# Performance work log

Measured on AMD Instinct MI355X. Metric: run time of the kernel, lower is better.

The kernel has to match this reference:

```python
import jax, jax.numpy as jnp
import numpy as np
import math

B, L, D, P = 2, 2048, 256, 32
PI = math.pi


def _layernorm(x, g, b, eps=1e-5):
    m = x.mean(-1, keepdims=True)
    v = x.var(-1, keepdims=True)
    return (x - m) / jnp.sqrt(v + eps) * g + b


def setup_inputs() -> dict:
    key = jax.random.key(0)
    ks = jax.random.split(key, 16)
    sd = 1.0 / math.sqrt(D)
    f32 = jnp.float32
    inp = {
        "x": jax.random.normal(ks[0], (B, L, D), f32),
        # key_encoder: Linear(D, P)
        "key_W": jax.random.normal(ks[1], (D, P), f32) * sd,
        "key_b": jnp.zeros((P,), f32),
        # value_encoder: Linear(D, D)
        "val_W": jax.random.normal(ks[2], (D, D), f32) * sd,
        "val_b": jnp.zeros((D,), f32),
        # refiner: LayerNorm(D), Linear(D, 2D), GELU, Linear(2D, D)
        "ln1_g": jnp.ones((D,), f32),
        "ln1_b": jnp.zeros((D,), f32),
        "W1": jax.random.normal(ks[3], (D, 2 * D), f32) * sd,
        "b1": jnp.zeros((2 * D,), f32),
        "W2": jax.random.normal(ks[4], (2 * D, D), f32) * (1.0 / math.sqrt(2 * D)),
        "b2": jnp.zeros((D,), f32),
        # to_out: LayerNorm(D), Linear(D, D)
        "ln2_g": jnp.ones((D,), f32),
        "ln2_b": jnp.zeros((D,), f32),
        "Wo": jax.random.normal(ks[5], (D, D), f32) * sd,
        "bo": jnp.zeros((D,), f32),
    }
    return inp


def reference(x, key_W, key_b, val_W, val_b, ln1_g, ln1_b, W1, b1, W2, b2,
              ln2_g, ln2_b, Wo, bo):
    # key phases in (-pi, pi); phasor exp(i*theta) handled as (cos, sin)
    phases = jnp.tanh(x @ key_W + key_b) * PI          # (B, L, P)
    values = x @ val_W + val_b                          # (B, L, D)

    cos_p = jnp.cos(phases)
    sin_p = jnp.sin(phases)
    # torch.roll(shifts=1, dims=1) then zero the first position -> shift right, row 0 = 0
    zrow = jnp.zeros_like(cos_p[:, :1])
    cos_s = jnp.concatenate([zrow, cos_p[:, :-1]], axis=1)
    sin_s = jnp.concatenate([zrow, sin_p[:, :-1]], axis=1)

    # odd positions hold values
    vmask = (jnp.arange(L) % 2 == 1).astype(x.dtype)    # (L,)
    mv = values * vmask[None, :, None]                  # (B, L, D)

    # bind: outer product phasor (P) x value (D); real/imag parts
    bound_re = cos_s[..., None] * mv[:, :, None, :]     # (B, L, P, D)
    bound_im = sin_s[..., None] * mv[:, :, None, :]
    mem_re = jnp.cumsum(bound_re, axis=1)
    mem_im = jnp.cumsum(bound_im, axis=1)

    # retrieve: Re[ memory * exp(-i*theta) ] summed over phases
    retrieved = (jnp.einsum('blpd,blp->bld', mem_re, cos_p)
                 + jnp.einsum('blpd,blp->bld', mem_im, sin_p))

    valid = jnp.maximum(jnp.cumsum(vmask), 1.0)         # (L,)
    retrieved = retrieved / (jnp.sqrt(valid)[None, :, None] * math.sqrt(P))

    h = _layernorm(retrieved, ln1_g, ln1_b)
    h = jax.nn.gelu(h @ W1 + b1, approximate=False)
    refined = h @ W2 + b2
    out = x + (_layernorm(refined, ln2_g, ln2_b) @ Wo + bo)
    return out
```

## Files before the change

### kernel.cpp

```cpp
#include <hip/hip_runtime.h>
#include <math.h>

#define BB 2
#define LL 2048
#define DD 256
#define PP 32
#define NC 64
#define PI_F 3.14159265358979323846f

typedef __attribute__((ext_vector_type(8))) short bf16x8;
typedef __attribute__((ext_vector_type(4))) float f32x4;
typedef unsigned short ushort_t;
typedef unsigned int uint_t;

__device__ inline ushort_t f2bf(float x) {
    uint_t u = __float_as_uint(x);
    uint_t r = (u + 0x7fffu + ((u >> 16) & 1u)) >> 16;
    return (ushort_t)r;
}

__global__ __launch_bounds__(256) void prep_key_kernel(
    const float* __restrict__ W1, const float* __restrict__ W2,
    const float* __restrict__ Wo, const float* __restrict__ valW,
    const float* __restrict__ x, const float* __restrict__ key_W,
    const float* __restrict__ key_b,
    ushort_t* __restrict__ W1t, ushort_t* __restrict__ W2t,
    ushort_t* __restrict__ Wot, ushort_t* __restrict__ valWt,
    float2* __restrict__ ph)
{
    const int bid = blockIdx.x;
    const int t = threadIdx.x;
    if (bid < 96) {
        __shared__ float T[64][65];
        const float* W; ushort_t* Wt; int K, N, tile;
        if (bid < 32)      { W = W1;   Wt = W1t;   K = 256; N = 512; tile = bid; }
        else if (bid < 64) { W = W2;   Wt = W2t;   K = 512; N = 256; tile = bid - 32; }
        else if (bid < 80) { W = Wo;   Wt = Wot;   K = 256; N = 256; tile = bid - 64; }
        else               { W = valW; Wt = valWt; K = 256; N = 256; tile = bid - 80; }
        const int ntiles = N / 64;
        const int k0 = (tile / ntiles) * 64, n0 = (tile % ntiles) * 64;
        {
            const int rr = t >> 2, cb = (t & 3) * 16;
            #pragma unroll
            for (int i = 0; i < 16; i += 4) {
                const float4 v = *(const float4*)&W[(k0 + rr) * N + n0 + cb + i];
                T[rr][cb + i + 0] = v.x; T[rr][cb + i + 1] = v.y;
                T[rr][cb + i + 2] = v.z; T[rr][cb + i + 3] = v.w;
            }
        }
        __syncthreads();
        {
            const int n = t >> 2, kb = (t & 3) * 16;
            #pragma unroll
            for (int i = 0; i < 16; ++i)
                Wt[(n0 + n) * K + k0 + kb + i] = f2bf(T[kb + i][n]);
        }
    } else {
        __shared__ float xs[256][8];
        __shared__ float kw[256][33];
        const int row0 = (bid - 96) * 8;
        #pragma unroll
        for (int i = 0; i < 8; ++i)
            xs[t][i] = x[(row0 + i) * DD + t];
        #pragma unroll
        for (int p4 = 0; p4 < 8; ++p4) {
            const int idx4 = p4 * 256 + t;
            const int k = idx4 >> 3, pc = (idx4 & 7) * 4;
            const float4 v = *(const float4*)&key_W[k * 32 + pc];
            kw[k][pc + 0] = v.x; kw[k][pc + 1] = v.y;
            kw[k][pc + 2] = v.z; kw[k][pc + 3] = v.w;
        }
        __syncthreads();
        const int r = t >> 5, p = t & 31;
        float a = key_b[p];
        #pragma unroll 8
        for (int k = 0; k < DD; ++k)
            a += xs[k][r] * kw[k][p];
        a = tanhf(a) * PI_F;
        float sn, cs;
        sincosf(a, &sn, &cs);
        ph[(row0 + r) * PP + p] = make_float2(cs, sn);
    }
}

__global__ __launch_bounds__(256) void valbind_kernel(
    const float* __restrict__ x, const float2* __restrict__ ph,
    const ushort_t* __restrict__ valWt, const float* __restrict__ val_b,
    ushort_t* __restrict__ VoddT, float* __restrict__ Mt)
{
    __shared__ ushort_t xsb[16][264];
    __shared__ ushort_t VdT[128][40];
    __shared__ ushort_t phsT[64][40];
    __shared__ float    Ms[128][68];

    const int tid = threadIdx.x;
    const int bid = blockIdx.x;
    const int b  = bid >> 7;
    const int rem = bid & 127;
    const int c  = rem >> 1;
    const int dh = rem & 1;
    const int base = b * LL;
    const int r0 = 32 * c;

    {
        const int j = tid >> 4, cb = (tid & 15) * 16;
        const float* src = &x[(long)(base + r0 + 2 * j + 1) * DD + cb];
        ushort_t tmp[16];
        #pragma unroll
        for (int i = 0; i < 4; ++i) {
            const float4 v = *(const float4*)&src[i * 4];
            tmp[i*4+0] = f2bf(v.x); tmp[i*4+1] = f2bf(v.y);
            tmp[i*4+2] = f2bf(v.z); tmp[i*4+3] = f2bf(v.w);
        }
        *(uint4*)&xsb[j][cb]     = *(uint4*)&tmp[0];
        *(uint4*)&xsb[j][cb + 8] = *(uint4*)&tmp[8];
    }
    {
        const int j = tid >> 4, qb = (tid & 15) * 4;
        const float4 v = *(const float4*)((const float*)ph +
                              (long)(base + r0 + 2 * j) * 64 + qb);
        phsT[qb + 0][j] = f2bf(v.x);
        phsT[qb + 1][j] = f2bf(v.y);
        phsT[qb + 2][j] = f2bf(v.z);
        phsT[qb + 3][j] = f2bf(v.w);
    }
    for (int e = tid; e < 64 * 16; e += 256)
        phsT[e >> 4][16 + (e & 15)] = 0;
    for (int e = tid; e < 128 * 16; e += 256)
        VdT[e >> 4][16 + (e & 15)] = 0;
    __syncthreads();

    const int wv = tid >> 6, lane = tid & 63;
    const int qd = lane >> 4, mc = lane & 15;

    f32x4 va0 = {0.f,0.f,0.f,0.f}, va1 = {0.f,0.f,0.f,0.f};
    const int dloc0 = wv * 32 + mc, dloc1 = dloc0 + 16;
    const int n0g = dh * 128 + dloc0, n1g = n0g + 16;
    const ushort_t* B0 = &valWt[(long)n0g * 256];
    const ushort_t* B1 = &valWt[(long)n1g * 256];
    #pragma unroll
    for (int ks = 0; ks < 8; ++ks) {
        const bf16x8 a  = *(const bf16x8*)&xsb[mc][ks * 32 + qd * 8];
        const bf16x8 b0 = *(const bf16x8*)&B0[ks * 32 + qd * 8];
        const bf16x8 b1 = *(const bf16x8*)&B1[ks * 32 + qd * 8];
        va0 = __builtin_amdgcn_mfma_f32_16x16x32_bf16(a, b0, va0, 0, 0, 0);
        va1 = __builtin_amdgcn_mfma_f32_16x16x32_bf16(a, b1, va1, 0, 0, 0);
    }
    {
        const float bb0 = val_b[n0g], bb1 = val_b[n1g];
        #pragma unroll
        for (int r = 0; r < 4; ++r) {
            const int j = qd * 4 + r;
            VdT[dloc0][j] = f2bf(va0[r] + bb0);
            VdT[dloc1][j] = f2bf(va1[r] + bb1);
        }
    }
    __syncthreads();

    const bf16x8 a2 = *(const bf16x8*)&phsT[wv * 16 + mc][qd * 8];
    f32x4 macc[8];
    #pragma unroll
    for (int nf = 0; nf < 8; ++nf) {
        f32x4 z = {0.f,0.f,0.f,0.f};
        const bf16x8 b2 = *(const bf16x8*)&VdT[nf * 16 + mc][qd * 8];
        macc[nf] = __builtin_amdgcn_mfma_f32_16x16x32_bf16(a2, b2, z, 0, 0, 0);
    }
    #pragma unroll
    for (int nf = 0; nf < 8; ++nf) {
        #pragma unroll
        for (int r = 0; r < 4; ++r) {
            const int q = wv * 16 + qd * 4 + r;
            Ms[nf * 16 + mc][q] = macc[nf][r];
        }
    }
    __syncthreads();

    {
        float* dst = &Mt[((long)(b * NC + c) * 256 + dh * 128) * 64];
        #pragma unroll
        for (int p = 0; p < 8; ++p) {
            const int idx4 = p * 256 + tid;
            const int dloc = idx4 >> 4, q4 = (idx4 & 15) * 4;
            const float4 v = *(const float4*)&Ms[dloc][q4];
            *(float4*)&dst[dloc * 64 + q4] = v;
        }
    }
    if (tid < 128) {
        ushort_t* vd = &VoddT[((long)(b * NC + c) * 256 + dh * 128 + tid) * 16];
        *(uint4*)&vd[0] = *(const uint4*)&VdT[tid][0];
        *(uint4*)&vd[8] = *(const uint4*)&VdT[tid][8];
    }
}

__global__ __launch_bounds__(256) void prefix_kernel(float* __restrict__ M)
{
    __shared__ float segsum[4][64];
    const int tid = threadIdx.x;
    const int b  = blockIdx.x >> 8;
    const int cg = blockIdx.x & 255;
    const int col = cg * 64 + (tid & 63);
    const int seg = tid >> 6;
    const long base = (long)b * NC * 16384 + col;

    float v[16], s = 0.f;
    #pragma unroll
    for (int i = 0; i < 16; ++i) {
        v[i] = M[base + (long)(seg * 16 + i) * 16384];
        s += v[i];
    }
    segsum[seg][tid & 63] = s;
    __syncthreads();
    float run = 0.f;
    #pragma unroll
    for (int sg = 0; sg < 3; ++sg)
        if (sg < seg) run += segsum[sg][tid & 63];
    #pragma unroll
    for (int i = 0; i < 16; ++i) {
        const long a = base + (long)(seg * 16 + i) * 16384;
        M[a] = run;
        run += v[i];
    }
}

__global__ __launch_bounds__(256) void retrieve_kernel(
    const float* __restrict__ ph, const float* __restrict__ Mpre,
    const ushort_t* __restrict__ VoddT,
    const float* __restrict__ ln1_g, const float* __restrict__ ln1_b,
    ushort_t* __restrict__ rhat)
{
    __shared__ ushort_t Bs_m[256][72];
    __shared__ ushort_t Bs_v[256][32];
    __shared__ ushort_t As_ph[16][72];
    __shared__ ushort_t Bs_sh[16][72];
    __shared__ ushort_t As_p[16][32];
    __shared__ float    ref[16][264];

    const int tid = threadIdx.x;
    const int b = blockIdx.x >> 7;
    const int c = (blockIdx.x >> 1) & 63;
    const int h = blockIdx.x & 1;
    const int l0g = 32 * c + 16 * h;
    const long rowbase = (long)b * LL + l0g;

    {
        const float* src = &Mpre[(long)(b * NC + c) * 16384];
        #pragma unroll
        for (int p = 0; p < 16; ++p) {
            const int idx4 = p * 256 + tid;
            const int d = idx4 >> 4, q4 = (idx4 & 15) * 4;
            const float4 v = *(const float4*)&src[idx4 * 4];
            ushort_t tmp[4] = {f2bf(v.x), f2bf(v.y), f2bf(v.z), f2bf(v.w)};
            *(uint2*)&Bs_m[d][q4] = *(uint2*)tmp;
        }
    }
    {
        const int r = tid >> 4, q4 = (tid & 15) * 4;
        const float4 v = *(const float4*)&ph[(rowbase + r) * 64 + q4];
        ushort_t t0[4] = {f2bf(v.x), f2bf(v.y), f2bf(v.z), f2bf(v.w)};
        *(uint2*)&As_ph[r][q4] = *(uint2*)t0;
        const float4 w = *(const float4*)&ph[((long)b * LL + 32 * c + 2 * r) * 64 + q4];
        ushort_t t1[4] = {f2bf(w.x), f2bf(w.y), f2bf(w.z), f2bf(w.w)};
        *(uint2*)&Bs_sh[r][q4] = *(uint2*)t1;
    }
    {
        const ushort_t* src = &VoddT[(long)(b * NC + c) * 4096];
        const int j0 = (tid & 1) * 8;
        *(uint4*)&Bs_v[tid >> 1][j0] = *(const uint4*)&src[tid * 8];
        *(uint4*)&Bs_v[(tid + 256) >> 1][j0] = *(const uint4*)&src[(tid + 256) * 8];
        *(uint4*)&Bs_v[tid][16] = make_uint4(0, 0, 0, 0);
        *(uint4*)&Bs_v[tid][24] = make_uint4(0, 0, 0, 0);
        As_p[tid >> 4][16 + (tid & 15)] = 0;
    }
    __syncthreads();

    const int wv = tid >> 6, lane = tid & 63;
    const int qd = lane >> 4, mc = lane & 15;

    {
        f32x4 sacc = {0.f, 0.f, 0.f, 0.f};
        #pragma unroll
        for (int ks = 0; ks < 2; ++ks) {
            const bf16x8 a  = *(const bf16x8*)&As_ph[mc][ks * 32 + qd * 8];
            const bf16x8 bb = *(const bf16x8*)&Bs_sh[mc][ks * 32 + qd * 8];
            sacc = __builtin_amdgcn_mfma_f32_16x16x32_bf16(a, bb, sacc, 0, 0, 0);
        }
        if (wv == 0) {
            #pragma unroll
            for (int r = 0; r < 4; ++r) {
                const int l = qd * 4 + r;
                As_p[l][mc] = (2 * mc + 1 <= 16 * h + l) ? f2bf(sacc[r])
                                                         : (ushort_t)0;
            }
        }
    }

    f32x4 acc[4];
    #pragma unroll
    for (int i = 0; i < 4; ++i) acc[i] = (f32x4){0.f, 0.f, 0.f, 0.f};
    #pragma unroll
    for (int i = 0; i < 4; ++i) {
        const int d0 = wv * 64 + i * 16;
        #pragma unroll
        for (int ks = 0; ks < 2; ++ks) {
            const bf16x8 a  = *(const bf16x8*)&As_ph[mc][ks * 32 + qd * 8];
            const bf16x8 bb = *(const bf16x8*)&Bs_m[d0 + mc][ks * 32 + qd * 8];
            acc[i] = __builtin_amdgcn_mfma_f32_16x16x32_bf16(a, bb, acc[i], 0, 0, 0);
        }
    }
    __syncthreads();

    {
        const bf16x8 a2 = *(const bf16x8*)&As_p[mc][qd * 8];
        #pragma unroll
        for (int i = 0; i < 4; ++i) {
            const int d0 = wv * 64 + i * 16;
            const bf16x8 b2 = *(const bf16x8*)&Bs_v[d0 + mc][qd * 8];
            acc[i] = __builtin_amdgcn_mfma_f32_16x16x32_bf16(a2, b2, acc[i], 0, 0, 0);
        }
    }

    #pragma unroll
    for (int r = 0; r < 4; ++r) {
        const int l = qd * 4 + r;
        int va = (l0g + l + 1) >> 1; if (va < 1) va = 1;
        const float sc = 0.17677669529663687f * rsqrtf((float)va);
        #pragma unroll
        for (int i = 0; i < 4; ++i)
            ref[l][wv * 64 + i * 16 + mc] = acc[i][r] * sc;
    }
    __syncthreads();

    {
        const int row = tid >> 4, cg = (tid & 15) * 16;
        float s = 0.f, sq = 0.f;
        #pragma unroll
        for (int i = 0; i < 16; ++i) {
            const float v = ref[row][cg + i];
            s += v; sq += v * v;
        }
        s += __shfl_xor(s, 1, 16);  sq += __shfl_xor(sq, 1, 16);
        s += __shfl_xor(s, 2, 16);  sq += __shfl_xor(sq, 2, 16);
        s += __shfl_xor(s, 4, 16);  sq += __shfl_xor(sq, 4, 16);
        s += __shfl_xor(s, 8, 16);  sq += __shfl_xor(sq, 8, 16);
        const float m = s * (1.f / 256.f);
        const float inv = rsqrtf(sq * (1.f / 256.f) - m * m + 1e-5f);
        ushort_t o16[16];
        #pragma unroll
        for (int i = 0; i < 16; ++i) {
            const int cc = cg + i;
            o16[i] = f2bf((ref[row][cc] - m) * inv * ln1_g[cc] + ln1_b[cc]);
        }
        ushort_t* dst = &rhat[(rowbase + row) * DD + cg];
        *(uint4*)&dst[0] = *(uint4*)&o16[0];
        *(uint4*)&dst[8] = *(uint4*)&o16[8];
    }
}

template<int K, int N, int MODE>
__global__ __launch_bounds__(256) void mfma_gemm(
    const ushort_t* __restrict__ A, const ushort_t* __restrict__ Bt,
    const float* __restrict__ bias, const float* __restrict__ resid,
    void* __restrict__ out)
{
    __shared__ ushort_t As[16][136];
    __shared__ ushort_t Bs[64][136];
    const int tid = threadIdx.x;
    const int mt = blockIdx.x & 255;
    const int nt = blockIdx.x >> 8;
    const int m0 = mt * 16, n0 = nt * 64;
    const int wv = tid >> 6, lane = tid & 63;
    const int qd = lane >> 4, mc = lane & 15;

    f32x4 acc = {0.f, 0.f, 0.f, 0.f};

    const int ar = tid >> 4, ak = (tid & 15) * 8;
    const int bn = tid >> 2, bk = (tid & 3) * 32;

    for (int k0 = 0; k0 < K; k0 += 128) {
        __syncthreads();
        *(uint4*)&As[ar][ak] = *(const uint4*)&A[(long)(m0 + ar) * K + k0 + ak];
        {
            const ushort_t* src = &Bt[(long)(n0 + bn) * K + k0 + bk];
            *(uint4*)&Bs[bn][bk +  0] = *(const uint4*)&src[0];
            *(uint4*)&Bs[bn][bk +  8] = *(const uint4*)&src[8];
            *(uint4*)&Bs[bn][bk + 16] = *(const uint4*)&src[16];
            *(uint4*)&Bs[bn][bk + 24] = *(const uint4*)&src[24];
        }
        __syncthreads();
        #pragma unroll
        for (int ko = 0; ko < 128; ko += 32) {
            const bf16x8 a = *(const bf16x8*)&As[mc][ko + qd * 8];
            const bf16x8 b = *(const bf16x8*)&Bs[wv * 16 + mc][ko + qd * 8];
            acc = __builtin_amdgcn_mfma_f32_16x16x32_bf16(a, b, acc, 0, 0, 0);
        }
    }

    const int nn = n0 + wv * 16 + mc;
    const float bb = bias[nn];
    #pragma unroll
    for (int r = 0; r < 4; ++r) {
        const long row = m0 + qd * 4 + r;
        float v = acc[r] + bb;
        if (MODE == 0) {
            v = 0.5f * v * (1.f + erff(v * 0.70710678118654752f));
            ((ushort_t*)out)[row * N + nn] = f2bf(v);
        } else {
            ((float*)out)[row * N + nn] = v + resid[row * N + nn];
        }
    }
}

__global__ __launch_bounds__(256) void gemm2ln_kernel(
    const ushort_t* __restrict__ h, const ushort_t* __restrict__ W2t,
    const float* __restrict__ b2, const float* __restrict__ ln2_g,
    const float* __restrict__ ln2_b, ushort_t* __restrict__ shat)
{
    __shared__ ushort_t As[16][72];
    __shared__ ushort_t Bs[256][72];
    __shared__ float Ct[16][264];

    const int tid = threadIdx.x;
    const int m0 = blockIdx.x * 16;
    const int wv = tid >> 6, lane = tid & 63;
    const int qd = lane >> 4, mc = lane & 15;

    f32x4 acc[4];
    #pragma unroll
    for (int nf = 0; nf < 4; ++nf) acc[nf] = (f32x4){0.f,0.f,0.f,0.f};

    const int sr = tid >> 3, sk = (tid & 7) * 8;

    for (int k0 = 0; k0 < 512; k0 += 64) {
        __syncthreads();
        if (tid < 128)
            *(uint4*)&As[sr][sk] = *(const uint4*)&h[(long)(m0 + sr) * 512 + k0 + sk];
        #pragma unroll
        for (int rr = 0; rr < 8; ++rr) {
            const int n = rr * 32 + (tid >> 3);
            *(uint4*)&Bs[n][sk] = *(const uint4*)&W2t[(long)n * 512 + k0 + sk];
        }
        __syncthreads();
        #pragma unroll
        for (int ks = 0; ks < 2; ++ks) {
            const bf16x8 a = *(const bf16x8*)&As[mc][ks * 32 + qd * 8];
            #pragma unroll
            for (int nf = 0; nf < 4; ++nf) {
                const bf16x8 b = *(const bf16x8*)&Bs[wv * 64 + nf * 16 + mc][ks * 32 + qd * 8];
                acc[nf] = __builtin_amdgcn_mfma_f32_16x16x32_bf16(a, b, acc[nf], 0, 0, 0);
            }
        }
    }

    #pragma unroll
    for (int nf = 0; nf < 4; ++nf) {
        const int n = wv * 64 + nf * 16 + mc;
        const float bb = b2[n];
        #pragma unroll
        for (int r = 0; r < 4; ++r)
            Ct[qd * 4 + r][n] = acc[nf][r] + bb;
    }
    __syncthreads();

    {
        const int row = tid >> 4, cg = (tid & 15) * 16;
        float s = 0.f, sq = 0.f;
        #pragma unroll
        for (int i = 0; i < 16; ++i) {
            const float v = Ct[row][cg + i];
            s += v; sq += v * v;
        }
        s  += __shfl_xor(s, 1, 16);  sq += __shfl_xor(sq, 1, 16);
        s  += __shfl_xor(s, 2, 16);  sq += __shfl_xor(sq, 2, 16);
        s  += __shfl_xor(s, 4, 16);  sq += __shfl_xor(sq, 4, 16);
        s  += __shfl_xor(s, 8, 16);  sq += __shfl_xor(sq, 8, 16);
        const float m = s * (1.f / 256.f);
        const float inv = rsqrtf(sq * (1.f / 256.f) - m * m + 1e-5f);
        #pragma unroll
        for (int i = 0; i < 16; ++i) {
            const int cc = cg + i;
            shat[(long)(m0 + row) * DD + cc] =
                f2bf((Ct[row][cc] - m) * inv * ln2_g[cc] + ln2_b[cc]);
        }
    }
}

extern "C" void kernel_launch(void* const* d_in, const int* in_sizes, int n_in,
                              void* d_out, int out_size, void* d_ws, size_t ws_size,
                              hipStream_t stream)
{
    const float* x     = (const float*)d_in[0];
    const float* key_W = (const float*)d_in[1];
    const float* key_b = (const float*)d_in[2];
    const float* val_W = (const float*)d_in[3];
    const float* val_b = (const float*)d_in[4];
    const float* ln1_g = (const float*)d_in[5];
    const float* ln1_b = (const float*)d_in[6];
    const float* W1    = (const float*)d_in[7];
    const float* b1    = (const float*)d_in[8];
    const float* W2    = (const float*)d_in[9];
    const float* b2    = (const float*)d_in[10];
    const float* ln2_g = (const float*)d_in[11];
    const float* ln2_b = (const float*)d_in[12];
    const float* Wo    = (const float*)d_in[13];
    const float* bo    = (const float*)d_in[14];
    float* outp = (float*)d_out;

    float* ws = (float*)d_ws;
    float*  ph      = ws;
    float*  Mt      = ws + 262144;
    ushort_t* VoddT = (ushort_t*)(Mt + 2097152);
    ushort_t* rhat_b = VoddT + 524288;
    ushort_t* W1t   = rhat_b + 1048576;
    ushort_t* W2t   = W1t + 131072;
    ushort_t* Wot   = W2t + 131072;
    ushort_t* valWt = Wot + 65536;
    ushort_t* h_b    = (ushort_t*)Mt;
    ushort_t* shat_b = (ushort_t*)(Mt + 1048576);

    prep_key_kernel<<<608, 256, 0, stream>>>(W1, W2, Wo, val_W, x, key_W, key_b,
                                             W1t, W2t, Wot, valWt, (float2*)ph);
    valbind_kernel<<<256, 256, 0, stream>>>(x, (const float2*)ph, valWt, val_b,
                                            VoddT, Mt);
    prefix_kernel<<<512, 256, 0, stream>>>(Mt);
    retrieve_kernel<<<256, 256, 0, stream>>>(ph, Mt, VoddT, ln1_g, ln1_b, rhat_b);
    mfma_gemm<256, 512, 0><<<256 * 8, 256, 0, stream>>>(rhat_b, W1t, b1, nullptr, h_b);
    gemm2ln_kernel<<<256, 256, 0, stream>>>(h_b, W2t, b2, ln2_g, ln2_b, shat_b);
    mfma_gemm<256, 256, 2><<<256 * 4, 256, 0, stream>>>(shat_b, Wot, bo, x, outp);
}
```

Baseline: 133.1 us.

## Use MFMA for key projection, split valbind wider, and use 32-row GEMM tiles

The key-phase projection in the prep kernel now runs on bf16 MFMA, with 16 rows per block and the K dimension split across waves and reduced in shared memory. This replaces the scalar fp32 dot-product loop and lowers bf16 precision for the phases. The valbind kernel now splits D into quarters instead of halves, doubling the grid to 512 blocks for more parallelism. The FFN and output GEMMs use 32-row M tiles with two accumulators, which halves B-tile reloads and the grid size.

```diff
diff --git a/kernel.cpp b/kernel.cpp
--- a/kernel.cpp
+++ b/kernel.cpp
@@ -56,30 +56,66 @@
                 Wt[(n0 + n) * K + k0 + kb + i] = f2bf(T[kb + i][n]);
         }
     } else {
-        __shared__ float xs[256][8];
-        __shared__ float kw[256][33];
-        const int row0 = (bid - 96) * 8;
-        #pragma unroll
-        for (int i = 0; i < 8; ++i)
-            xs[t][i] = x[(row0 + i) * DD + t];
-        #pragma unroll
-        for (int p4 = 0; p4 < 8; ++p4) {
-            const int idx4 = p4 * 256 + t;
-            const int k = idx4 >> 3, pc = (idx4 & 7) * 4;
-            const float4 v = *(const float4*)&key_W[k * 32 + pc];
-            kw[k][pc + 0] = v.x; kw[k][pc + 1] = v.y;
-            kw[k][pc + 2] = v.z; kw[k][pc + 3] = v.w;
-        }
-        __syncthreads();
-        const int r = t >> 5, p = t & 31;
-        float a = key_b[p];
-        #pragma unroll 8
-        for (int k = 0; k < DD; ++k)
-            a += xs[k][r] * kw[k][p];
-        a = tanhf(a) * PI_F;
-        float sn, cs;
-        sincosf(a, &sn, &cs);
-        ph[(row0 + r) * PP + p] = make_float2(cs, sn);
+        __shared__ ushort_t xt[16][264];
+        __shared__ ushort_t kwT[32][264];
+        __shared__ float rbuf[4][2][16][17];
+        const int row0 = (bid - 96) * 16;
+        {
+            const int l = t >> 4, cb = (t & 15) * 16;
+            const float* src = &x[(long)(row0 + l) * DD + cb];
+            ushort_t tmp[16];
+            #pragma unroll
+            for (int i = 0; i < 4; ++i) {
+                const float4 v = *(const float4*)&src[i * 4];
+                tmp[i*4+0] = f2bf(v.x); tmp[i*4+1] = f2bf(v.y);
+                tmp[i*4+2] = f2bf(v.z); tmp[i*4+3] = f2bf(v.w);
+            }
+            *(uint4*)&xt[l][cb]     = *(uint4*)&tmp[0];
+            *(uint4*)&xt[l][cb + 8] = *(uint4*)&tmp[8];
+        }
+        {
+            #pragma unroll
+            for (int i = 0; i < 8; ++i) {
+                const int idx4 = i * 256 + t;
+                const int k = idx4 >> 3, pc = (idx4 & 7) * 4;
+                const float4 v = *(const float4*)&key_W[k * 32 + pc];
+                kwT[pc + 0][k] = f2bf(v.x);
+                kwT[pc + 1][k] = f2bf(v.y);
+                kwT[pc + 2][k] = f2bf(v.z);
+                kwT[pc + 3][k] = f2bf(v.w);
+            }
+        }
+        __syncthreads();
+        const int wv = t >> 6, lane = t & 63;
+        const int qd = lane >> 4, mc = lane & 15;
+        f32x4 acc0 = {0.f,0.f,0.f,0.f}, acc1 = {0.f,0.f,0.f,0.f};
+        #pragma unroll
+        for (int ks = 0; ks < 2; ++ks) {
+            const int ko = wv * 64 + ks * 32 + qd * 8;
+            const bf16x8 a  = *(const bf16x8*)&xt[mc][ko];
+            const bf16x8 b0 = *(const bf16x8*)&kwT[mc][ko];
+            const bf16x8 b1 = *(const bf16x8*)&kwT[16 + mc][ko];
+            acc0 = __builtin_amdgcn_mfma_f32_16x16x32_bf16(a, b0, acc0, 0, 0, 0);
+            acc1 = __builtin_amdgcn_mfma_f32_16x16x32_bf16(a, b1, acc1, 0, 0, 0);
+        }
+        #pragma unroll
+        for (int r = 0; r < 4; ++r) {
+            rbuf[wv][0][qd * 4 + r][mc] = acc0[r];
+            rbuf[wv][1][qd * 4 + r][mc] = acc1[r];
+        }
+        __syncthreads();
+        #pragma unroll
+        for (int rep = 0; rep < 2; ++rep) {
+            const int idx = rep * 256 + t;
+            const int p = idx & 31, l = idx >> 5;
+            const int nf = p >> 4, mcol = p & 15;
+            float a = key_b[p] + rbuf[0][nf][l][mcol] + rbuf[1][nf][l][mcol]
+                    + rbuf[2][nf][l][mcol] + rbuf[3][nf][l][mcol];
+            a = tanhf(a) * PI_F;
+            float sn, cs;
+            sincosf(a, &sn, &cs);
+            ph[(long)(row0 + l) * PP + p] = make_float2(cs, sn);
+        }
     }
 }
 
@@ -89,16 +125,15 @@
     ushort_t* __restrict__ VoddT, float* __restrict__ Mt)
 {
     __shared__ ushort_t xsb[16][264];
-    __shared__ ushort_t VdT[128][40];
+    __shared__ ushort_t VdT[64][40];
     __shared__ ushort_t phsT[64][40];
-    __shared__ float    Ms[128][68];
+    __shared__ float    Ms[64][68];
 
     const int tid = threadIdx.x;
     const int bid = blockIdx.x;
-    const int b  = bid >> 7;
-    const int rem = bid & 127;
-    const int c  = rem >> 1;
-    const int dh = rem & 1;
+    const int b  = bid >> 8;
+    const int c  = (bid >> 2) & 63;
+    const int dq = bid & 3;
     const int base = b * LL;
     const int r0 = 32 * c;
 
@@ -124,69 +159,60 @@
         phsT[qb + 2][j] = f2bf(v.z);
         phsT[qb + 3][j] = f2bf(v.w);
     }
-    for (int e = tid; e < 64 * 16; e += 256)
+    for (int e = tid; e < 64 * 16; e += 256) {
         phsT[e >> 4][16 + (e & 15)] = 0;
-    for (int e = tid; e < 128 * 16; e += 256)
         VdT[e >> 4][16 + (e & 15)] = 0;
+    }
     __syncthreads();
 
     const int wv = tid >> 6, lane = tid & 63;
     const int qd = lane >> 4, mc = lane & 15;
 
-    f32x4 va0 = {0.f,0.f,0.f,0.f}, va1 = {0.f,0.f,0.f,0.f};
-    const int dloc0 = wv * 32 + mc, dloc1 = dloc0 + 16;
-    const int n0g = dh * 128 + dloc0, n1g = n0g + 16;
-    const ushort_t* B0 = &valWt[(long)n0g * 256];
-    const ushort_t* B1 = &valWt[(long)n1g * 256];
+    f32x4 va = {0.f,0.f,0.f,0.f};
+    const int dloc = wv * 16 + mc;
+    const int ng = dq * 64 + dloc;
+    const ushort_t* B0 = &valWt[(long)ng * 256];
     #pragma unroll
     for (int ks = 0; ks < 8; ++ks) {
         const bf16x8 a  = *(const bf16x8*)&xsb[mc][ks * 32 + qd * 8];
         const bf16x8 b0 = *(const bf16x8*)&B0[ks * 32 + qd * 8];
-        const bf16x8 b1 = *(const bf16x8*)&B1[ks * 32 + qd * 8];
-        va0 = __builtin_amdgcn_mfma_f32_16x16x32_bf16(a, b0, va0, 0, 0, 0);
-        va1 = __builtin_amdgcn_mfma_f32_16x16x32_bf16(a, b1, va1, 0, 0, 0);
-    }
-    {
-        const float bb0 = val_b[n0g], bb1 = val_b[n1g];
-        #pragma unroll
-        for (int r = 0; r < 4; ++r) {
-            const int j = qd * 4 + r;
-            VdT[dloc0][j] = f2bf(va0[r] + bb0);
-            VdT[dloc1][j] = f2bf(va1[r] + bb1);
-        }
+        va = __builtin_amdgcn_mfma_f32_16x16x32_bf16(a, b0, va, 0, 0, 0);
+    }
+    {
+        const float bb = val_b[ng];
+        #pragma unroll
+        for (int r = 0; r < 4; ++r)
+            VdT[dloc][qd * 4 + r] = f2bf(va[r] + bb);
     }
     __syncthreads();
 
     const bf16x8 a2 = *(const bf16x8*)&phsT[wv * 16 + mc][qd * 8];
-    f32x4 macc[8];
-    #pragma unroll
-    for (int nf = 0; nf < 8; ++nf) {
+    f32x4 macc[4];
+    #pragma unroll
+    for (int nf = 0; nf < 4; ++nf) {
         f32x4 z = {0.f,0.f,0.f,0.f};
         const bf16x8 b2 = *(const bf16x8*)&VdT[nf * 16 + mc][qd * 8];
         macc[nf] = __builtin_amdgcn_mfma_f32_16x16x32_bf16(a2, b2, z, 0, 0, 0);
     }
     #pragma unroll
-    for (int nf = 0; nf < 8; ++nf) {
-        #pragma unroll
-        for (int r = 0; r < 4; ++r) {
-            const int q = wv * 16 + qd * 4 + r;
-            Ms[nf * 16 + mc][q] = macc[nf][r];
-        }
-    }
-    __syncthreads();
-
-    {
-        float* dst = &Mt[((long)(b * NC + c) * 256 + dh * 128) * 64];
-        #pragma unroll
-        for (int p = 0; p < 8; ++p) {
+    for (int nf = 0; nf < 4; ++nf) {
+        #pragma unroll
+        for (int r = 0; r < 4; ++r)
+            Ms[nf * 16 + mc][wv * 16 + qd * 4 + r] = macc[nf][r];
+    }
+    __syncthreads();
+
+    {
+        float* dst = &Mt[((long)(b * NC + c) * 256 + dq * 64) * 64];
+        #pragma unroll
+        for (int p = 0; p < 4; ++p) {
             const int idx4 = p * 256 + tid;
-            const int dloc = idx4 >> 4, q4 = (idx4 & 15) * 4;
-            const float4 v = *(const float4*)&Ms[dloc][q4];
-            *(float4*)&dst[dloc * 64 + q4] = v;
-        }
-    }
-    if (tid < 128) {
-        ushort_t* vd = &VoddT[((long)(b * NC + c) * 256 + dh * 128 + tid) * 16];
+            const int dl = idx4 >> 4, q4 = (idx4 & 15) * 4;
+            *(float4*)&dst[dl * 64 + q4] = *(const float4*)&Ms[dl][q4];
+        }
+    }
+    if (tid < 64) {
+        ushort_t* vd = &VoddT[((long)(b * NC + c) * 256 + dq * 64 + tid) * 16];
         *(uint4*)&vd[0] = *(const uint4*)&VdT[tid][0];
         *(uint4*)&vd[8] = *(const uint4*)&VdT[tid][8];
     }
@@ -357,28 +383,33 @@
 }
 
 template<int K, int N, int MODE>
-__global__ __launch_bounds__(256) void mfma_gemm(
+__global__ __launch_bounds__(256) void mfma_gemm32(
     const ushort_t* __restrict__ A, const ushort_t* __restrict__ Bt,
     const float* __restrict__ bias, const float* __restrict__ resid,
     void* __restrict__ out)
 {
-    __shared__ ushort_t As[16][136];
+    __shared__ ushort_t As[32][136];
     __shared__ ushort_t Bs[64][136];
     const int tid = threadIdx.x;
-    const int mt = blockIdx.x & 255;
-    const int nt = blockIdx.x >> 8;
-    const int m0 = mt * 16, n0 = nt * 64;
+    const int mt = blockIdx.x & 127;
+    const int nt = blockIdx.x >> 7;
+    const int m0 = mt * 32, n0 = nt * 64;
     const int wv = tid >> 6, lane = tid & 63;
     const int qd = lane >> 4, mc = lane & 15;
 
-    f32x4 acc = {0.f, 0.f, 0.f, 0.f};
-
-    const int ar = tid >> 4, ak = (tid & 15) * 8;
+    f32x4 acc0 = {0.f, 0.f, 0.f, 0.f};
+    f32x4 acc1 = {0.f, 0.f, 0.f, 0.f};
+
+    const int ar = tid >> 3, ak = (tid & 7) * 16;
     const int bn = tid >> 2, bk = (tid & 3) * 32;
 
     for (int k0 = 0; k0 < K; k0 += 128) {
         __syncthreads();
-        *(uint4*)&As[ar][ak] = *(const uint4*)&A[(long)(m0 + ar) * K + k0 + ak];
+        {
+            const ushort_t* sa = &A[(long)(m0 + ar) * K + k0 + ak];
+            *(uint4*)&As[ar][ak]     = *(const uint4*)&sa[0];
+            *(uint4*)&As[ar][ak + 8] = *(const uint4*)&sa[8];
+        }
         {
             const ushort_t* src = &Bt[(long)(n0 + bn) * K + k0 + bk];
             *(uint4*)&Bs[bn][bk +  0] = *(const uint4*)&src[0];
@@ -389,9 +420,11 @@
         __syncthreads();
         #pragma unroll
         for (int ko = 0; ko < 128; ko += 32) {
-            const bf16x8 a = *(const bf16x8*)&As[mc][ko + qd * 8];
-            const bf16x8 b = *(const bf16x8*)&Bs[wv * 16 + mc][ko + qd * 8];
-            acc = __builtin_amdgcn_mfma_f32_16x16x32_bf16(a, b, acc, 0, 0, 0);
+            const bf16x8 a0 = *(const bf16x8*)&As[mc][ko + qd * 8];
+            const bf16x8 a1 = *(const bf16x8*)&As[16 + mc][ko + qd * 8];
+            const bf16x8 b  = *(const bf16x8*)&Bs[wv * 16 + mc][ko + qd * 8];
+            acc0 = __builtin_amdgcn_mfma_f32_16x16x32_bf16(a0, b, acc0, 0, 0, 0);
+            acc1 = __builtin_amdgcn_mfma_f32_16x16x32_bf16(a1, b, acc1, 0, 0, 0);
         }
     }
 
@@ -399,13 +432,18 @@
     const float bb = bias[nn];
     #pragma unroll
     for (int r = 0; r < 4; ++r) {
-        const long row = m0 + qd * 4 + r;
-        float v = acc[r] + bb;
+        const long row0w = m0 + qd * 4 + r;
+        const long row1w = row0w + 16;
+        float v0 = acc0[r] + bb;
+        float v1 = acc1[r] + bb;
         if (MODE == 0) {
-            v = 0.5f * v * (1.f + erff(v * 0.70710678118654752f));
-            ((ushort_t*)out)[row * N + nn] = f2bf(v);
+            v0 = 0.5f * v0 * (1.f + erff(v0 * 0.70710678118654752f));
+            v1 = 0.5f * v1 * (1.f + erff(v1 * 0.70710678118654752f));
+            ((ushort_t*)out)[row0w * N + nn] = f2bf(v0);
+            ((ushort_t*)out)[row1w * N + nn] = f2bf(v1);
         } else {
-            ((float*)out)[row * N + nn] = v + resid[row * N + nn];
+            ((float*)out)[row0w * N + nn] = v0 + resid[row0w * N + nn];
+            ((float*)out)[row1w * N + nn] = v1 + resid[row1w * N + nn];
         }
     }
 }
@@ -517,13 +555,13 @@
     ushort_t* h_b    = (ushort_t*)Mt;
     ushort_t* shat_b = (ushort_t*)(Mt + 1048576);
 
-    prep_key_kernel<<<608, 256, 0, stream>>>(W1, W2, Wo, val_W, x, key_W, key_b,
+    prep_key_kernel<<<352, 256, 0, stream>>>(W1, W2, Wo, val_W, x, key_W, key_b,
                                              W1t, W2t, Wot, valWt, (float2*)ph);
-    valbind_kernel<<<256, 256, 0, stream>>>(x, (const float2*)ph, valWt, val_b,
+    valbind_kernel<<<512, 256, 0, stream>>>(x, (const float2*)ph, valWt, val_b,
                                             VoddT, Mt);
     prefix_kernel<<<512, 256, 0, stream>>>(Mt);
     retrieve_kernel<<<256, 256, 0, stream>>>(ph, Mt, VoddT, ln1_g, ln1_b, rhat_b);
-    mfma_gemm<256, 512, 0><<<256 * 8, 256, 0, stream>>>(rhat_b, W1t, b1, nullptr, h_b);
+    mfma_gemm32<256, 512, 0><<<1024, 256, 0, stream>>>(rhat_b, W1t, b1, nullptr, h_b);
     gemm2ln_kernel<<<256, 256, 0, stream>>>(h_b, W2t, b2, ln2_g, ln2_b, shat_b);
-    mfma_gemm<256, 256, 2><<<256 * 4, 256, 0, stream>>>(shat_b, Wot, bo, x, outp);
-}
+    mfma_gemm32<256, 256, 2><<<512, 256, 0, stream>>>(shat_b, Wot, bo, x, outp);
+}
```

Result: faster. 130.4 us (-2.1%).
